# Performance work log

Measured on AMD Instinct MI355X. Metric: run time of the kernel, lower is better.

## Reference

```python
import jax, jax.numpy as jnp
import numpy as np

STRIDE = 1
PADDING = 1
THRESHOLD = 0.5
NAN_FRAC = 0.05


def _conv(x, k, stride):
    return jax.lax.conv_general_dilated(
        x, k, (stride, stride), 'VALID',
        dimension_numbers=('NCHW', 'OIHW', 'NCHW'))


def setup_inputs() -> dict:
    key = jax.random.key(0)
    k1, k2, k3, k4 = jax.random.split(key, 4)
    B, C, H, W = 16, 128, 128, 128
    OC, KH, KW = 256, 3, 3
    x = jax.random.normal(k1, (B, C, H, W), jnp.float32)
    nan_mask = jax.random.uniform(k2, (B, C, H, W)) < NAN_FRAC
    x = jnp.where(nan_mask, jnp.nan, x)
    kernel = jax.random.normal(k3, (OC, C, KH, KW), jnp.float32) * 0.05
    bias = jax.random.normal(k4, (OC,), jnp.float32) * 0.05
    return {"x": x, "kernel": kernel, "bias": bias}


def reference(x, kernel, bias):
    # NaN-aware conv: per-patch nan stats shared across out_channels.
    p = PADDING
    x = jnp.pad(x, ((0, 0), (0, 0), (p, p), (p, p)))  # zero pad (zeros are valid values)
    mask = jnp.isnan(x)
    x0 = jnp.where(mask, jnp.zeros((), x.dtype), x)
    OC, C, KH, KW = kernel.shape
    total = float(C * KH * KW)
    ones = jnp.ones((1, C, KH, KW), x.dtype)
    maskf = mask.astype(x.dtype)
    nan_count = _conv(maskf, ones, STRIDE)      # [B,1,oh,ow]
    val_sum = _conv(x0, ones, STRIDE)           # sum of non-nan values per patch
    valid = total - nan_count
    patch_mean = val_sum / jnp.maximum(valid, 1.0)
    s1 = _conv(x0, kernel, STRIDE)              # conv with NaNs zeroed
    m = _conv(maskf, kernel, STRIDE)            # sum of kernel weights at NaN positions
    out = s1 + patch_mean * m + bias[None, :, None, None]
    bad = nan_count / total >= THRESHOLD        # includes all-NaN patches
    return jnp.where(bad, jnp.nan, out)
```

## Files before the change

### kernel.cpp

```cpp
#include <hip/hip_runtime.h>


typedef __attribute__((ext_vector_type(8))) short bf16x8;
typedef __attribute__((ext_vector_type(4))) float f32x4;

#define HH 128
#define WW 128
#define CC 128

__device__ __forceinline__ unsigned short f2bf(float f) {
    union { float f; unsigned int i; } v; v.f = f;
    unsigned int u = v.i;
    if ((u & 0x7FFFFFFFu) > 0x7F800000u) return (unsigned short)((u >> 16) | 0x0040u);
    unsigned int r = u + 0x7FFFu + ((u >> 16) & 1u);
    return (unsigned short)(r >> 16);
}
__device__ __forceinline__ unsigned int sel2(unsigned int v, unsigned int pmu) {
    unsigned int lo = v & 0xFFFFu, hi = v >> 16;
    if ((lo & 0x7FFFu) > 0x7F80u) lo = pmu;
    if ((hi & 0x7FFFu) > 0x7F80u) hi = pmu;
    return lo | (hi << 16);
}

__global__ void k_transpose_stats(const float* __restrict__ x,
                                  unsigned short* __restrict__ xT,
                                  float* __restrict__ cnt,
                                  float* __restrict__ sum, int b0) {
    int bh = blockIdx.x;
    int bl = bh >> 7, h = bh & 127;
    int b = b0 + bl;
    int w = threadIdx.x;
    const float* xp = x + ((long)b * CC * HH * WW) + h * WW + w;
    unsigned short* xTp = xT + ((((long)bh << 7) + w) << 7);
    int cntv = 0; float sumv = 0.f;
    for (int c8 = 0; c8 < 16; ++c8) {
        unsigned short s8[8];
        #pragma unroll
        for (int j = 0; j < 8; ++j) {
            float fv = xp[(long)(c8 * 8 + j) * (HH * WW)];
            unsigned int bits = __float_as_uint(fv);
            if ((bits & 0x7FFFFFFFu) > 0x7F800000u) { cntv++; s8[j] = 0x7FC0u; }
            else { sumv += fv; s8[j] = f2bf(fv); }
        }
        uint4 p;
        p.x = (unsigned)s8[0] | ((unsigned)s8[1] << 16);
        p.y = (unsigned)s8[2] | ((unsigned)s8[3] << 16);
        p.z = (unsigned)s8[4] | ((unsigned)s8[5] << 16);
        p.w = (unsigned)s8[6] | ((unsigned)s8[7] << 16);
        *(uint4*)(xTp + c8 * 8) = p;
    }
    cnt[(bh << 7) + w] = (float)cntv;
    sum[(bh << 7) + w] = sumv;
}

__global__ void k_patchmean(const float* __restrict__ cnt, const float* __restrict__ sum,
                            unsigned short* __restrict__ pm) {
    int idx = blockIdx.x * 256 + threadIdx.x;
    int ow = idx & 127, oh = (idx >> 7) & 127, bl = idx >> 14;
    float nc = 0.f, vs = 0.f;
    #pragma unroll
    for (int kh = 0; kh < 3; ++kh) {
        int ih = oh + kh - 1; if (ih < 0 || ih >= HH) continue;
        #pragma unroll
        for (int kw = 0; kw < 3; ++kw) {
            int iw = ow + kw - 1; if (iw < 0 || iw >= WW) continue;
            int p = (((bl << 7) + ih) << 7) + iw;
            nc += cnt[p]; vs += sum[p];
        }
    }
    float pmv = vs / fmaxf(1152.f - nc, 1.f);
    unsigned short r = f2bf(pmv);
    if (nc >= 576.f) r = 0x7FC0u;
    pm[idx] = r;
}

__global__ void k_w2(const float* __restrict__ krn, unsigned short* __restrict__ W2) {
    int e = blockIdx.x * 256 + threadIdx.x;
    int c = e & 127, oc = (e >> 7) & 255, khw = e >> 15;
    W2[e] = f2bf(krn[(oc * 128 + c) * 9 + khw]);
}

__global__ __launch_bounds__(256) void k_gemm(
    const unsigned short* __restrict__ xT, const unsigned short* __restrict__ pm,
    const unsigned short* __restrict__ W2, const float* __restrict__ bias,
    float* __restrict__ out, int b0) {
    __shared__ __align__(16) unsigned short lA[128 * 72];
    __shared__ __align__(16) unsigned short lB[128 * 72];
    int bid = blockIdx.x;
    int nt = bid & 1;
    int mtl = bid >> 1;
    int bl = mtl >> 7, oh = mtl & 127;
    int b = b0 + bl;
    int oc0 = nt << 7;
    int tid = threadIdx.x;
    int lane = tid & 63, wave = tid >> 6;
    int wm = wave >> 1, wn = wave & 1;
    int l15 = lane & 15, quad = lane >> 4;

    int sr = tid >> 1;
    int sc = (tid & 1) * 32;
    unsigned int pmr = pm[(mtl << 7) + sr];

    f32x4 acc[4][4];
    #pragma unroll
    for (int i = 0; i < 4; ++i)
        #pragma unroll
        for (int j = 0; j < 4; ++j) acc[i][j] = (f32x4)0.f;

    for (int kh = 0; kh < 3; ++kh) {
        int ih = oh + kh - 1;
        if (ih < 0 || ih >= HH) continue;
        for (int kw = 0; kw < 3; ++kw) {
            int iw = sr + kw - 1;
            bool inb = (iw >= 0 && iw < WW);
            const unsigned short* ap = xT + (((((bl << 7) + ih) << 7) + iw) << 7) + sc;
            int khw = kh * 3 + kw;
            const unsigned short* bp = W2 + (((khw << 8) + oc0 + sr) << 7) + sc;
            for (int c0 = 0; c0 < 128; c0 += 64) {
                __syncthreads();
                unsigned short* la = &lA[sr * 72 + sc];
                if (inb) {
                    #pragma unroll
                    for (int i = 0; i < 4; ++i) {
                        uint4 v = *(const uint4*)(ap + c0 + i * 8);
                        uint4 r;
                        r.x = sel2(v.x, pmr); r.y = sel2(v.y, pmr);
                        r.z = sel2(v.z, pmr); r.w = sel2(v.w, pmr);
                        *(uint4*)(la + i * 8) = r;
                    }
                } else {
                    uint4 z; z.x = 0; z.y = 0; z.z = 0; z.w = 0;
                    #pragma unroll
                    for (int i = 0; i < 4; ++i) *(uint4*)(la + i * 8) = z;
                }
                unsigned short* lb = &lB[sr * 72 + sc];
                #pragma unroll
                for (int i = 0; i < 4; ++i)
                    *(uint4*)(lb + i * 8) = *(const uint4*)(bp + c0 + i * 8);
                __syncthreads();
                #pragma unroll
                for (int ks = 0; ks < 2; ++ks) {
                    bf16x8 af[4], bfr[4];
                    #pragma unroll
                    for (int mi = 0; mi < 4; ++mi)
                        af[mi] = *(const bf16x8*)&lA[((wm << 6) + (mi << 4) + l15) * 72 + (ks << 5) + (quad << 3)];
                    #pragma unroll
                    for (int ni = 0; ni < 4; ++ni)
                        bfr[ni] = *(const bf16x8*)&lB[((wn << 6) + (ni << 4) + l15) * 72 + (ks << 5) + (quad << 3)];
                    #pragma unroll
                    for (int mi = 0; mi < 4; ++mi)
                        #pragma unroll
                        for (int ni = 0; ni < 4; ++ni)
                            acc[mi][ni] = __builtin_amdgcn_mfma_f32_16x16x32_bf16(
                                af[mi], bfr[ni], acc[mi][ni], 0, 0, 0);
                }
            }
        }
    }

    #pragma unroll
    for (int ni = 0; ni < 4; ++ni) {
        int oc = oc0 + (wn << 6) + (ni << 4) + l15;
        float bv = bias[oc];
        float* op = out + ((long)((b << 8) + oc) * 128 + oh) * 128;
        #pragma unroll
        for (int mi = 0; mi < 4; ++mi) {
            int ow0 = (wm << 6) + (mi << 4) + (quad << 2);
            float4 o;
            o.x = acc[mi][ni][0] + bv;
            o.y = acc[mi][ni][1] + bv;
            o.z = acc[mi][ni][2] + bv;
            o.w = acc[mi][ni][3] + bv;
            *(float4*)(op + ow0) = o;
        }
    }
}

extern "C" void kernel_launch(void* const* d_in, const int* in_sizes, int n_in,
                              void* d_out, int out_size, void* d_ws, size_t ws_size,
                              hipStream_t stream) {
    const float* x    = (const float*)d_in[0];
    const float* krn  = (const float*)d_in[1];
    const float* bias = (const float*)d_in[2];
    float* out = (float*)d_out;

    const size_t W2_BYTES = 294912ull * 2;
    int G = 16;
    while (G > 1) {
        size_t need = W2_BYTES + 256
                    + (size_t)G * (16384ull * 128 * 2)
                    + (size_t)G * (16384ull * 4) * 2
                    + (size_t)G * (16384ull * 2)
                    + 1024;
        if (need <= ws_size) break;
        G >>= 1;
    }

    char* ws = (char*)d_ws;
    size_t off = 0;
    auto carve = [&](size_t bytes) { char* p = ws + off; off += (bytes + 255) & ~255ull; return p; };
    unsigned short* W2  = (unsigned short*)carve(W2_BYTES);
    unsigned short* xT  = (unsigned short*)carve((size_t)G * 16384 * 128 * 2);
    float*          cnt = (float*)carve((size_t)G * 16384 * 4);
    float*          sum = (float*)carve((size_t)G * 16384 * 4);
    unsigned short* pm  = (unsigned short*)carve((size_t)G * 16384 * 2);

    k_w2<<<dim3(1152), dim3(256), 0, stream>>>(krn, W2);
    for (int b0 = 0; b0 < 16; b0 += G) {
        k_transpose_stats<<<dim3(G * 128), dim3(128), 0, stream>>>(x, xT, cnt, sum, b0);
        k_patchmean<<<dim3(G * 64), dim3(256), 0, stream>>>(cnt, sum, pm);
        k_gemm<<<dim3(G * 256), dim3(256), 0, stream>>>(xT, pm, W2, bias, out, b0);
    }
}
```

Measured before the change: 737.1 us.

## Double-buffer GEMM LDS stages with direct global-to-LDS weight loads and swizzle

Reworks the conv GEMM kernel so each block covers 64 output pixels by all 256 output channels, instead of 128 pixels by 128 channels. Weights are pre-swizzled in k_w2 and copied straight into LDS with global_load_lds. The A tile is stored with an XOR swizzle in place of the padded layout. Two LDS buffers let the next stage's loads overlap the current stage's MFMAs, halving the barriers per stage. In exchange, LDS use grows to roughly 80 KB per block, which may lower occupancy, and the reshaped tile changes how much weight and activation data each block reuses.

```diff
diff --git a/kernel.cpp b/kernel.cpp
--- a/kernel.cpp
+++ b/kernel.cpp
@@ -20,6 +20,11 @@
     if ((lo & 0x7FFFu) > 0x7F80u) lo = pmu;
     if ((hi & 0x7FFFu) > 0x7F80u) hi = pmu;
     return lo | (hi << 16);
+}
+__device__ __forceinline__ void gl16(const void* g, void* l) {
+    __builtin_amdgcn_global_load_lds(
+        (const __attribute__((address_space(1))) unsigned int*)g,
+        (__attribute__((address_space(3))) unsigned int*)l, 16, 0, 0);
 }
 
 __global__ void k_transpose_stats(const float* __restrict__ x,
@@ -76,30 +81,38 @@
 
 __global__ void k_w2(const float* __restrict__ krn, unsigned short* __restrict__ W2) {
     int e = blockIdx.x * 256 + threadIdx.x;
-    int c = e & 127, oc = (e >> 7) & 255, khw = e >> 15;
-    W2[e] = f2bf(krn[(oc * 128 + c) * 9 + khw]);
+    int s = e & 63;
+    int r = (e >> 6) & 255;
+    int half = (e >> 14) & 1;
+    int khw = e >> 15;
+    int c = (half << 6) | (s ^ ((r & 7) << 3));
+    W2[e] = f2bf(krn[(r * 128 + c) * 9 + khw]);
 }
 
 __global__ __launch_bounds__(256) void k_gemm(
     const unsigned short* __restrict__ xT, const unsigned short* __restrict__ pm,
     const unsigned short* __restrict__ W2, const float* __restrict__ bias,
     float* __restrict__ out, int b0) {
-    __shared__ __align__(16) unsigned short lA[128 * 72];
-    __shared__ __align__(16) unsigned short lB[128 * 72];
+    __shared__ __align__(16) unsigned short lA[2][64 * 64];
+    __shared__ __align__(16) unsigned short lB[2][256 * 64];
+
     int bid = blockIdx.x;
-    int nt = bid & 1;
-    int mtl = bid >> 1;
-    int bl = mtl >> 7, oh = mtl & 127;
-    int b = b0 + bl;
-    int oc0 = nt << 7;
+    int ow0 = (bid & 1) << 6;
+    int oh  = (bid >> 1) & 127;
+    int bl  = bid >> 8;
+    int b   = b0 + bl;
+
     int tid = threadIdx.x;
     int lane = tid & 63, wave = tid >> 6;
-    int wm = wave >> 1, wn = wave & 1;
     int l15 = lane & 15, quad = lane >> 4;
 
-    int sr = tid >> 1;
-    int sc = (tid & 1) * 32;
-    unsigned int pmr = pm[(mtl << 7) + sr];
+    int arow = tid >> 2, apart = tid & 3;
+    int ow = ow0 + arow;
+    unsigned int pmr = pm[(((bl << 7) + oh) << 7) + ow];
+
+    const char* w2base = (const char*)W2;
+    int bgoff = (wave << 13) + (lane << 4);
+    int bloff = (wave << 13);
 
     f32x4 acc[4][4];
     #pragma unroll
@@ -107,71 +120,83 @@
         #pragma unroll
         for (int j = 0; j < 4; ++j) acc[i][j] = (f32x4)0.f;
 
-    for (int kh = 0; kh < 3; ++kh) {
-        int ih = oh + kh - 1;
-        if (ih < 0 || ih >= HH) continue;
-        for (int kw = 0; kw < 3; ++kw) {
-            int iw = sr + kw - 1;
-            bool inb = (iw >= 0 && iw < WW);
-            const unsigned short* ap = xT + (((((bl << 7) + ih) << 7) + iw) << 7) + sc;
-            int khw = kh * 3 + kw;
-            const unsigned short* bp = W2 + (((khw << 8) + oc0 + sr) << 7) + sc;
-            for (int c0 = 0; c0 < 128; c0 += 64) {
-                __syncthreads();
-                unsigned short* la = &lA[sr * 72 + sc];
-                if (inb) {
-                    #pragma unroll
-                    for (int i = 0; i < 4; ++i) {
-                        uint4 v = *(const uint4*)(ap + c0 + i * 8);
-                        uint4 r;
-                        r.x = sel2(v.x, pmr); r.y = sel2(v.y, pmr);
-                        r.z = sel2(v.z, pmr); r.w = sel2(v.w, pmr);
-                        *(uint4*)(la + i * 8) = r;
-                    }
-                } else {
-                    uint4 z; z.x = 0; z.y = 0; z.z = 0; z.w = 0;
-                    #pragma unroll
-                    for (int i = 0; i < 4; ++i) *(uint4*)(la + i * 8) = z;
-                }
-                unsigned short* lb = &lB[sr * 72 + sc];
+    auto STAGE = [&](unsigned short* la, unsigned short* lb, int s) {
+        int khw = s >> 1, c0 = (s & 1) << 6;
+        int kh = khw / 3, kw = khw - kh * 3;
+        int ih = oh + kh - 1, iw = ow + kw - 1;
+        const char* bsrc = w2base + (s << 15) + bgoff;
+        char* ldst = (char*)lb + bloff;
+        #pragma unroll
+        for (int i = 0; i < 8; ++i)
+            gl16(bsrc + (i << 10), ldst + (i << 10));
+        uint4 v0 = {0u,0u,0u,0u}, v1 = {0u,0u,0u,0u};
+        if ((unsigned)ih < 128u && (unsigned)iw < 128u) {
+            const unsigned short* ap =
+                xT + ((((long)((bl << 7) + ih) << 7) + iw) << 7) + c0 + (apart << 4);
+            v0 = *(const uint4*)ap;
+            v1 = *(const uint4*)(ap + 8);
+        }
+        uint4 r0, r1;
+        r0.x = sel2(v0.x, pmr); r0.y = sel2(v0.y, pmr);
+        r0.z = sel2(v0.z, pmr); r0.w = sel2(v0.w, pmr);
+        r1.x = sel2(v1.x, pmr); r1.y = sel2(v1.y, pmr);
+        r1.z = sel2(v1.z, pmr); r1.w = sel2(v1.w, pmr);
+        char* lar = (char*)la + (arow << 7);
+        int sw = (arow & 7) << 4;
+        *(uint4*)(lar + (((apart << 5) | 0)  ^ sw)) = r0;
+        *(uint4*)(lar + (((apart << 5) | 16) ^ sw)) = r1;
+    };
+
+    auto COMPUTE = [&](const unsigned short* la, const unsigned short* lb) {
+        int swr = (l15 & 7) << 4;
+        #pragma unroll
+        for (int ks = 0; ks < 2; ++ks) {
+            bf16x8 af[4], bfr[4];
+            int cb = ((ks << 6) | (quad << 4)) ^ swr;
+            #pragma unroll
+            for (int mi = 0; mi < 4; ++mi) {
+                int r = (mi << 4) + l15;
+                af[mi] = *(const bf16x8*)((const char*)la + (r << 7) + cb);
+            }
+            #pragma unroll
+            for (int ni = 0; ni < 4; ++ni) {
+                int r = (wave << 6) + (ni << 4) + l15;
+                bfr[ni] = *(const bf16x8*)((const char*)lb + (r << 7) + cb);
+            }
+            #pragma unroll
+            for (int mi = 0; mi < 4; ++mi)
                 #pragma unroll
-                for (int i = 0; i < 4; ++i)
-                    *(uint4*)(lb + i * 8) = *(const uint4*)(bp + c0 + i * 8);
-                __syncthreads();
-                #pragma unroll
-                for (int ks = 0; ks < 2; ++ks) {
-                    bf16x8 af[4], bfr[4];
-                    #pragma unroll
-                    for (int mi = 0; mi < 4; ++mi)
-                        af[mi] = *(const bf16x8*)&lA[((wm << 6) + (mi << 4) + l15) * 72 + (ks << 5) + (quad << 3)];
-                    #pragma unroll
-                    for (int ni = 0; ni < 4; ++ni)
-                        bfr[ni] = *(const bf16x8*)&lB[((wn << 6) + (ni << 4) + l15) * 72 + (ks << 5) + (quad << 3)];
-                    #pragma unroll
-                    for (int mi = 0; mi < 4; ++mi)
-                        #pragma unroll
-                        for (int ni = 0; ni < 4; ++ni)
-                            acc[mi][ni] = __builtin_amdgcn_mfma_f32_16x16x32_bf16(
-                                af[mi], bfr[ni], acc[mi][ni], 0, 0, 0);
-                }
-            }
-        }
+                for (int ni = 0; ni < 4; ++ni)
+                    acc[mi][ni] = __builtin_amdgcn_mfma_f32_16x16x32_bf16(
+                        af[mi], bfr[ni], acc[mi][ni], 0, 0, 0);
+        }
+    };
+
+    STAGE(lA[0], lB[0], 0);
+    __syncthreads();
+    for (int s = 0; s < 18; s += 2) {
+        STAGE(lA[1], lB[1], s + 1);
+        COMPUTE(lA[0], lB[0]);
+        __syncthreads();
+        if (s + 2 < 18) STAGE(lA[0], lB[0], s + 2);
+        COMPUTE(lA[1], lB[1]);
+        __syncthreads();
     }
 
     #pragma unroll
     for (int ni = 0; ni < 4; ++ni) {
-        int oc = oc0 + (wn << 6) + (ni << 4) + l15;
+        int oc = (wave << 6) + (ni << 4) + l15;
         float bv = bias[oc];
-        float* op = out + ((long)((b << 8) + oc) * 128 + oh) * 128;
+        float* op = out + ((long)((b << 8) + oc) * 128 + oh) * 128 + ow0;
         #pragma unroll
         for (int mi = 0; mi < 4; ++mi) {
-            int ow0 = (wm << 6) + (mi << 4) + (quad << 2);
+            int og = (mi << 4) + (quad << 2);
             float4 o;
             o.x = acc[mi][ni][0] + bv;
             o.y = acc[mi][ni][1] + bv;
             o.z = acc[mi][ni][2] + bv;
             o.w = acc[mi][ni][3] + bv;
-            *(float4*)(op + ow0) = o;
+            *(float4*)(op + og) = o;
         }
     }
 }
```

Result: faster. 672.9 us (-8.7%).
